# Kernel optimization log

Hardware: AMD Instinct MI355X
Metric: run time of the kernel (lower is better)

Reference implementation:

```python
import jax, jax.numpy as jnp
import numpy as np

# config (mirrors the original `config` module)
V = 50257   # vocab_size
E = 512     # embedding dim
H = 1024    # hidden size
S = 128     # encoder length
B = 8       # config.beam_size
T = 64      # config.MAX_LENGTH
SOS = 1
EOS = 2
NEG = -1e9


def setup_inputs() -> dict:
    key = jax.random.key(0)
    ks = jax.random.split(key, 7)
    s = jnp.float32(0.05)
    return {
        "emb": jax.random.normal(ks[0], (V, E), jnp.float32) * s,
        "Wx": jax.random.normal(ks[1], (E, 3 * H), jnp.float32) * s,
        "Wh": jax.random.normal(ks[2], (H, 3 * H), jnp.float32) * s,
        "W_out": jax.random.normal(ks[3], (2 * H, V), jnp.float32) * s,
        "b_out": jax.random.normal(ks[4], (V,), jnp.float32) * s,
        "enc": jax.random.normal(ks[5], (S, H), jnp.float32) * s,
        "h0": jax.random.normal(ks[6], (H,), jnp.float32) * s,
    }


def _gru(x, h, Wx, Wh):
    gx = x @ Wx
    gh = h @ Wh
    xz, xr, xn = jnp.split(gx, 3, axis=-1)
    hz, hr, hn = jnp.split(gh, 3, axis=-1)
    z = jax.nn.sigmoid(xz + hz)
    r = jax.nn.sigmoid(xr + hr)
    n = jnp.tanh(xn + r * hn)
    return (1.0 - z) * n + z * h


def _beam_search(emb, Wx, Wh, W_out, b_out, enc, h0):
    def step(carry, step_idx):
        tokens, cum, length, finished, latest, h = carry
        # decoder step for all live beams at once (batch = B)
        x = emb[latest]                               # [B, E]
        h_new = _gru(x, h, Wx, Wh)                    # [B, H]
        att = jax.nn.softmax(h_new @ enc.T, axis=-1)  # [B, S]
        ctx = att @ enc                               # [B, H]
        logits = jnp.concatenate([h_new, ctx], axis=-1) @ W_out + b_out
        logp = jax.nn.log_softmax(logits, axis=-1)    # [B, V] == log(probs)
        tk_lp, tk_id = jax.lax.top_k(logp, B)         # per-beam topk(beam_size)

        alive = ~finished
        # candidate cumulative log-probs and lengths (length counts SOS, as in avg_log_prob)
        cand_cum = cum[:, None] + jnp.where(alive[:, None], tk_lp, 0.0)   # [B, B]
        cand_len = length[:, None] + alive[:, None].astype(jnp.int32)    # [B, B]
        cand_score = cand_cum / cand_len.astype(cand_cum.dtype)          # avg_log_prob
        # finished beams contribute a single frozen candidate (their result slot)
        valid = alive[:, None] | (jnp.arange(B)[None, :] == 0)
        # steps == 0: num_old_beams = 1 (only beam 0 expands)
        valid = valid & ((step_idx > 0) | (jnp.arange(B)[:, None] == 0))
        flat = jnp.where(valid, cand_score, NEG).reshape(-1)             # [B*B]
        _, top_idx = jax.lax.top_k(flat, B)           # sort_beams + keep beam_size
        parent = top_idx // B
        child = top_idx % B

        p_fin = finished[parent]
        p_len = length[parent]
        new_tok = tk_id[parent, child]                # [B]
        # append new token at position (len - 1) unless parent already finished
        pos = (jnp.arange(T)[None, :] == (p_len - 1)[:, None]) & (~p_fin)[:, None]
        tokens_n = jnp.where(pos, new_tok[:, None], tokens[parent])
        fin_n = p_fin | (new_tok == EOS)
        cum_n = cand_cum.reshape(-1)[top_idx]
        len_n = cand_len.reshape(-1)[top_idx]
        latest_n = jnp.where(p_fin, latest[parent], new_tok)
        return (tokens_n, cum_n, len_n, fin_n, latest_n, h_new[parent]), None

    tokens0 = jnp.zeros((B, T), jnp.int32)
    cum0 = jnp.zeros((B,), jnp.float32)       # log_probs = [0.0] for SOS
    len0 = jnp.ones((B,), jnp.int32)          # tokens = [SOS]
    fin0 = jnp.zeros((B,), bool)
    latest0 = jnp.full((B,), SOS, jnp.int32)
    h_init = jnp.tile(h0[None, :], (B, 1))
    carry = (tokens0, cum0, len0, fin0, latest0, h_init)
    (tokens, cum, length, finished, _, _), _ = jax.lax.scan(step, carry, jnp.arange(T))

    score = cum / length.astype(cum.dtype)
    # prefer finished (EOS) beams, else fall back to live beams, best avg_log_prob
    adj = jnp.where(jnp.any(finished), jnp.where(finished, score, NEG), score)
    best = jnp.argmax(adj)
    return tokens[best], score[best]


def reference(emb, Wx, Wh, W_out, b_out, enc, h0):
    return _beam_search(emb, Wx, Wh, W_out, b_out, enc, h0)
```

## Files before the change

### kernel.cpp

```cpp
#include <hip/hip_runtime.h>
#include <math.h>

#define V    50257
#define E    512
#define H    1024
#define S    128
#define BS   8
#define T    64
#define SOS  1
#define EOS  2
#define NEGV (-1e9f)
#define H3   (3*H)
#define KS   16
#define RPK  ((E+H)/KS)
#define TKCH 6283
#define CB   197

__global__ void k_init(const float* __restrict__ h0, float* h, float* cum,
                       int* len, int* fin, int* lat, int* tok) {
    int t = threadIdx.x;
    for (int i = t; i < BS*H; i += 256) h[i] = h0[i % H];
    for (int i = t; i < BS*T; i += 256) tok[i] = 0;
    if (t < BS) { cum[t] = 0.f; len[t] = 1; fin[t] = 0; lat[t] = SOS; }
}

__global__ __launch_bounds__(256) void k_gru_part(
    const float* __restrict__ emb, const float* __restrict__ Wx,
    const float* __restrict__ Wh, const float* __restrict__ h,
    const int* __restrict__ lat, float* __restrict__ part)
{
    int jb = blockIdx.x;
    int k  = blockIdx.y;
    int t  = threadIdx.x;
    int j  = jb*256 + t;
    int c0 = k * RPK;
    __shared__ float vals[RPK*BS];
    for (int m = t; m < RPK*8; m += 256) {
        int c = c0 + (m >> 3);
        int b = m & 7;
        float v;
        if (c < E) v = emb[(size_t)lat[b]*E + c];
        else       v = h[b*H + (c - E)];
        vals[m] = v;
    }
    __syncthreads();
    float pz[BS] = {0}, pr[BS] = {0}, pnx[BS] = {0}, pnh[BS] = {0};
    for (int cc = 0; cc < RPK; ++cc) {
        int c = c0 + cc;
        bool isx = (c < E);
        const float* Wrow = isx ? (Wx + (size_t)c*H3) : (Wh + (size_t)(c-E)*H3);
        float wz = Wrow[j];
        float wr = Wrow[j + H];
        float wn = Wrow[j + 2*H];
        #pragma unroll
        for (int b = 0; b < BS; ++b) {
            float v = vals[cc*8 + b];
            pz[b] += v * wz;
            pr[b] += v * wr;
            if (isx) pnx[b] += v * wn; else pnh[b] += v * wn;
        }
    }
    #pragma unroll
    for (int b = 0; b < BS; ++b) {
        part[(((size_t)k*4 + 0)*8 + b)*H + j] = pz[b];
        part[(((size_t)k*4 + 1)*8 + b)*H + j] = pr[b];
        part[(((size_t)k*4 + 2)*8 + b)*H + j] = pnx[b];
        part[(((size_t)k*4 + 3)*8 + b)*H + j] = pnh[b];
    }
}

__global__ __launch_bounds__(256) void k_gate_attn(
    const float* __restrict__ part, const float* __restrict__ h,
    const float* __restrict__ enc, float* __restrict__ hcT)
{
    int b = blockIdx.x;
    int t = threadIdx.x;
    __shared__ float hn[H];
    __shared__ float att[S];
    __shared__ float smax, ssum;
    for (int j = t; j < H; j += 256) {
        float pz = 0.f, pr = 0.f, pnx = 0.f, pnh = 0.f;
        #pragma unroll
        for (int k = 0; k < KS; ++k) {
            pz  += part[(((size_t)k*4 + 0)*8 + b)*H + j];
            pr  += part[(((size_t)k*4 + 1)*8 + b)*H + j];
            pnx += part[(((size_t)k*4 + 2)*8 + b)*H + j];
            pnh += part[(((size_t)k*4 + 3)*8 + b)*H + j];
        }
        float z = 1.f / (1.f + expf(-pz));
        float r = 1.f / (1.f + expf(-pr));
        float n = tanhf(pnx + r * pnh);
        float v = (1.f - z) * n + z * h[b*H + j];
        hn[j] = v;
        hcT[(size_t)j*8 + b] = v;
    }
    __syncthreads();
    int wave = t >> 6, lane = t & 63;
    for (int s = wave; s < S; s += 4) {
        float acc = 0.f;
        #pragma unroll 4
        for (int hh = lane; hh < H; hh += 64)
            acc += hn[hh] * enc[(size_t)s*H + hh];
        #pragma unroll
        for (int off = 32; off; off >>= 1) acc += __shfl_down(acc, off, 64);
        if (lane == 0) att[s] = acc;
    }
    __syncthreads();
    if (t == 0) {
        float m = -3.0e38f;
        for (int s = 0; s < S; ++s) m = fmaxf(m, att[s]);
        smax = m;
    }
    __syncthreads();
    if (t < S) att[t] = expf(att[t] - smax);
    __syncthreads();
    if (t == 0) {
        float sum = 0.f;
        for (int s = 0; s < S; ++s) sum += att[s];
        ssum = sum;
    }
    __syncthreads();
    if (t < S) att[t] = att[t] / ssum;
    __syncthreads();
    for (int j = t; j < H; j += 256) {
        float acc = 0.f;
        for (int s = 0; s < S; ++s) acc += att[s] * enc[(size_t)s*H + j];
        hcT[(size_t)(H + j)*8 + b] = acc;
    }
}

__global__ __launch_bounds__(256) void k_gemv_part(
    const float* __restrict__ Wout, const float* __restrict__ hcT,
    float* __restrict__ lpart)
{
    int t  = threadIdx.x;
    int rs = blockIdx.y;
    int r0 = rs * 256;
    int c  = blockIdx.x * 256 + t;
    __shared__ float hc[256*8];
    for (int m = t; m < 256*8; m += 256) hc[m] = hcT[(size_t)r0*8 + m];
    __syncthreads();
    int cl = (c < V) ? c : (V - 1);
    const float* wp = Wout + (size_t)r0*V + cl;
    float a[8] = {0,0,0,0,0,0,0,0};
    #pragma unroll 8
    for (int rr = 0; rr < 256; ++rr) {
        float w = wp[(size_t)rr*V];
        const float* hr = hc + rr*8;
        #pragma unroll
        for (int b = 0; b < 8; ++b) a[b] += hr[b] * w;
    }
    if (c < V) {
        #pragma unroll
        for (int b = 0; b < 8; ++b)
            lpart[((size_t)rs*8 + b)*V + c] = a[b];
    }
}

__global__ __launch_bounds__(256) void k_topk_part(
    const float* __restrict__ lpart, const float* __restrict__ bout,
    float* __restrict__ cand_v, int* __restrict__ cand_i,
    float* __restrict__ cm, float* __restrict__ clp)
{
    int b = blockIdx.x, c = blockIdx.y, t = threadIdx.x;
    int vstart = c * TKCH;
    int vend = (vstart + TKCH < V) ? (vstart + TKCH) : V;
    float bv[8]; int bi[8];
    #pragma unroll
    for (int r = 0; r < 8; ++r) { bv[r] = -3.0e38f; bi[r] = 0x7fffffff; }
    float m = -3.0e38f, l = 0.f;
    for (int v = vstart + t; v < vend; v += 256) {
        float x = bout[v];
        #pragma unroll
        for (int r = 0; r < 8; ++r)
            x += lpart[((size_t)r*8 + b)*V + v];
        if (x > m) { l = l * expf(m - x) + 1.f; m = x; }
        else         l += expf(x - m);
        if (x > bv[7]) {
            bv[7] = x; bi[7] = v;
            #pragma unroll
            for (int q = 7; q > 0; --q) {
                if (bv[q] > bv[q-1]) {
                    float tv = bv[q]; bv[q] = bv[q-1]; bv[q-1] = tv;
                    int   ti = bi[q]; bi[q] = bi[q-1]; bi[q-1] = ti;
                }
            }
        }
    }
    __shared__ float pm[256], pl[256];
    pm[t] = m; pl[t] = l;
    __syncthreads();
    for (int off = 128; off; off >>= 1) {
        if (t < off) {
            float m2 = pm[t+off], l2 = pl[t+off];
            float M = fmaxf(pm[t], m2);
            pl[t] = pl[t]*expf(pm[t]-M) + l2*expf(m2-M);
            pm[t] = M;
        }
        __syncthreads();
    }
    if (t == 0) { cm[b*8 + c] = pm[0]; clp[b*8 + c] = pl[0]; }

    __shared__ float pv[2048];
    __shared__ int   pi[2048];
    __shared__ float rv[256];
    __shared__ int   ri[256], rp[256];
    #pragma unroll
    for (int r = 0; r < 8; ++r) { pv[t*8+r] = bv[r]; pi[t*8+r] = bi[r]; }
    __syncthreads();
    for (int round = 0; round < 8; ++round) {
        float lv = -3.0e38f; int li = 0x7fffffff, lp = -1;
        #pragma unroll
        for (int r = 0; r < 8; ++r) {
            float v2 = pv[t*8+r]; int i2 = pi[t*8+r];
            if (v2 > lv || (v2 == lv && i2 < li)) { lv = v2; li = i2; lp = t*8+r; }
        }
        rv[t] = lv; ri[t] = li; rp[t] = lp;
        __syncthreads();
        for (int off = 128; off; off >>= 1) {
            if (t < off) {
                if (rv[t+off] > rv[t] || (rv[t+off] == rv[t] && ri[t+off] < ri[t])) {
                    rv[t] = rv[t+off]; ri[t] = ri[t+off]; rp[t] = rp[t+off];
                }
            }
            __syncthreads();
        }
        if (t == 0) {
            cand_v[(b*8 + c)*8 + round] = rv[0];
            cand_i[(b*8 + c)*8 + round] = ri[0];
            pv[rp[0]] = -3.0e38f; pi[rp[0]] = 0x7fffffff;
        }
        __syncthreads();
    }
}

__global__ __launch_bounds__(256) void k_merge_update_fb(
    const float* __restrict__ cand_v, const int* __restrict__ cand_i,
    const float* __restrict__ cm, const float* __restrict__ clp,
    const float* cum_i, const int* len_i, const int* fin_i,
    const int* lat_i, const int* tok_i,
    float* cum_o, int* len_o, int* fin_o, int* lat_o, int* tok_o,
    const float* __restrict__ hcT, float* __restrict__ h, int step)
{
    int t = threadIdx.x;
    __shared__ float cv[512];
    __shared__ int   ci[512];
    __shared__ float t8v[64];
    __shared__ int   t8i[64];
    __shared__ float lse[8];
    for (int i = t; i < 512; i += 256) { cv[i] = cand_v[i]; ci[i] = cand_i[i]; }
    __syncthreads();
    if (t < 8) {
        int b = t;
        float m = -3.0e38f, l = 0.f;
        for (int c = 0; c < 8; ++c) {
            float m2 = cm[b*8 + c], l2 = clp[b*8 + c];
            float M = fmaxf(m, m2);
            l = l*expf(m - M) + l2*expf(m2 - M);
            m = M;
        }
        lse[b] = m + logf(l);
        unsigned long long tk = 0ull;
        for (int round = 0; round < 8; ++round) {
            float bvv = -3.4e38f; int bii = 0x7fffffff, bp = 0;
            for (int i = 0; i < 64; ++i) {
                if ((tk >> i) & 1ull) continue;
                float v2 = cv[b*64 + i]; int i2 = ci[b*64 + i];
                if (v2 > bvv || (v2 == bvv && i2 < bii)) { bvv = v2; bii = i2; bp = i; }
            }
            tk |= 1ull << bp;
            t8v[b*8 + round] = bvv;
            t8i[b*8 + round] = bii;
        }
    }
    __syncthreads();

    __shared__ float flat[64];
    __shared__ float ccum[64];
    __shared__ int   clen[64];
    __shared__ int   sel[8];
    if (t < 64) {
        int b = t >> 3, j = t & 7;
        int alive = fin_i[b] ? 0 : 1;
        float lp = t8v[b*8 + j] - lse[b];
        float cc = cum_i[b] + (alive ? lp : 0.f);
        int   cln = len_i[b] + alive;
        float score = cc / (float)cln;
        bool valid = (alive || j == 0) && ((step > 0) || (b == 0));
        flat[t] = valid ? score : NEGV;
        ccum[t] = cc; clen[t] = cln;
    }
    __syncthreads();
    if (t == 0) {
        unsigned long long tk = 0ull;
        for (int r = 0; r < 8; ++r) {
            float bestv = -3.4e38f; int bidx = 0;
            for (int i = 0; i < 64; ++i) {
                if (!((tk >> i) & 1ull) && flat[i] > bestv) { bestv = flat[i]; bidx = i; }
            }
            tk |= 1ull << bidx; sel[r] = bidx;
        }
    }
    __syncthreads();
    if (t < 8) {
        int idx = sel[t];
        int parent = idx >> 3, child = idx & 7;
        int p_fin = fin_i[parent];
        int new_tok = t8i[parent*8 + child];
        cum_o[t] = ccum[idx];
        len_o[t] = clen[idx];
        fin_o[t] = (p_fin || new_tok == EOS) ? 1 : 0;
        lat_o[t] = p_fin ? lat_i[parent] : new_tok;
    }
    __syncthreads();
    for (int m = t; m < BS*T; m += 256) {
        int nb = m / T, pos = m % T;
        int idx = sel[nb];
        int parent = idx >> 3, child = idx & 7;
        int p_fin = fin_i[parent];
        int p_len = len_i[parent];
        int new_tok = t8i[parent*8 + child];
        int val = tok_i[parent*T + pos];
        if (pos == p_len - 1 && !p_fin) val = new_tok;
        tok_o[m] = val;
    }
    for (int m = t; m < BS*H; m += 256) {
        int nb = m / H, j = m % H;
        int parent = sel[nb] >> 3;
        h[m] = hcT[(size_t)j*8 + parent];
    }
}

__global__ void k_final(const float* cum, const int* len, const int* fin,
                        const int* tok, float* out)
{
    int t = threadIdx.x;
    __shared__ int bestIdx;
    if (t == 0) {
        bool anyf = false;
        for (int b = 0; b < BS; ++b) anyf = anyf || (fin[b] != 0);
        float bestv = -3.4e38f; int bi_ = 0;
        for (int b = 0; b < BS; ++b) {
            float sc = cum[b] / (float)len[b];
            float adj = anyf ? (fin[b] ? sc : NEGV) : sc;
            if (adj > bestv) { bestv = adj; bi_ = b; }
        }
        bestIdx = bi_;
        out[T] = cum[bi_] / (float)len[bi_];
    }
    __syncthreads();
    if (t < T) out[t] = (float)tok[bestIdx*T + t];
}

extern "C" void kernel_launch(void* const* d_in, const int* in_sizes, int n_in,
                              void* d_out, int out_size, void* d_ws, size_t ws_size,
                              hipStream_t stream) {
    const float* emb  = (const float*)d_in[0];
    const float* Wx   = (const float*)d_in[1];
    const float* Wh   = (const float*)d_in[2];
    const float* Wout = (const float*)d_in[3];
    const float* bout = (const float*)d_in[4];
    const float* enc  = (const float*)d_in[5];
    const float* h0   = (const float*)d_in[6];
    float* out = (float*)d_out;

    char* w = (char*)d_ws;
    auto alloc = [&](size_t bytes) -> char* {
        char* p = w; w += (bytes + 255) & ~(size_t)255; return p;
    };

    float* h      = (float*)alloc((size_t)BS*H*4);
    float* hcT    = (float*)alloc((size_t)2*H*BS*4);
    float* part   = (float*)alloc((size_t)KS*4*BS*H*4);
    float* cumb0  = (float*)alloc(8*4);
    float* cumb1  = (float*)alloc(8*4);
    int* lenb0 = (int*)alloc(8*4);
    int* lenb1 = (int*)alloc(8*4);
    int* finb0 = (int*)alloc(8*4);
    int* finb1 = (int*)alloc(8*4);
    int* latb0 = (int*)alloc(8*4);
    int* latb1 = (int*)alloc(8*4);
    int* tokb0 = (int*)alloc((size_t)BS*T*4);
    int* tokb1 = (int*)alloc((size_t)BS*T*4);

    float* lpart  = (float*)alloc((size_t)8*BS*V*4);
    float* cand_v = (float*)alloc(8*8*8*4);
    int*   cand_i = (int*)  alloc(8*8*8*4);
    float* cm     = (float*)alloc(64*4);
    float* clp    = (float*)alloc(64*4);

    float* cumb[2] = {cumb0, cumb1};
    int*   lenb[2] = {lenb0, lenb1};
    int*   finb[2] = {finb0, finb1};
    int*   latb[2] = {latb0, latb1};
    int*   tokb[2] = {tokb0, tokb1};

    k_init<<<1, 256, 0, stream>>>(h0, h, cumb[0], lenb[0], finb[0], latb[0], tokb[0]);

    for (int s = 0; s < T; ++s) {
        int p = s & 1, q = 1 - p;
        k_gru_part<<<dim3(4, KS), 256, 0, stream>>>(emb, Wx, Wh, h, latb[p], part);
        k_gate_attn<<<BS, 256, 0, stream>>>(part, h, enc, hcT);
        k_gemv_part<<<dim3(CB, 8), 256, 0, stream>>>(Wout, hcT, lpart);
        k_gemv_part<<<dim3(CB, 8), 256, 0, stream>>>(Wout, hcT, lpart);
        k_topk_part<<<dim3(BS, 8), 256, 0, stream>>>(lpart, bout, cand_v, cand_i, cm, clp);
        k_merge_update_fb<<<1, 256, 0, stream>>>(cand_v, cand_i, cm, clp,
                                                 cumb[p], lenb[p], finb[p], latb[p], tokb[p],
                                                 cumb[q], lenb[q], finb[q], latb[q], tokb[q],
                                                 hcT, h, s);
    }
    k_final<<<1, 64, 0, stream>>>(cumb[0], lenb[0], finb[0], tokb[0], out);
}
```

Before: 26.80 ms.

## Fuse beam-search steps into one cooperative persistent kernel with grid syncs

Replaces the per-step chain of kernel launches with a single cooperative kernel that runs all 64 decode steps and separates stages with grid-wide syncs. It keeps a multi-kernel fallback if the cooperative launch fails. It also drops the duplicated output GEMV launch, splits the context computation out of the attention stage so it runs across 32 blocks instead of 8, and uses nontemporal loads for W_out. The aim is to remove launch overhead and redundant work, at the cost of many grid barriers per step. Stages with few blocks, such as merge, leave most of the grid idle.

New measurement: 61.89 ms. 2.31x slower.

```diff
diff --git a/kernel.cpp b/kernel.cpp
--- a/kernel.cpp
+++ b/kernel.cpp
@@ -1,5 +1,8 @@
 #include <hip/hip_runtime.h>
+#include <hip/hip_cooperative_groups.h>
 #include <math.h>
+
+namespace cg = cooperative_groups;
 
 #define V    50257
 #define E    512
@@ -15,32 +18,37 @@
 #define RPK  ((E+H)/KS)
 #define TKCH 6283
 #define CB   197
-
-__global__ void k_init(const float* __restrict__ h0, float* h, float* cum,
-                       int* len, int* fin, int* lat, int* tok) {
-    int t = threadIdx.x;
-    for (int i = t; i < BS*H; i += 256) h[i] = h0[i % H];
-    for (int i = t; i < BS*T; i += 256) tok[i] = 0;
-    if (t < BS) { cum[t] = 0.f; len[t] = 1; fin[t] = 0; lat[t] = SOS; }
-}
-
-__global__ __launch_bounds__(256) void k_gru_part(
-    const float* __restrict__ emb, const float* __restrict__ Wx,
-    const float* __restrict__ Wh, const float* __restrict__ h,
-    const int* __restrict__ lat, float* __restrict__ part)
-{
-    int jb = blockIdx.x;
-    int k  = blockIdx.y;
-    int t  = threadIdx.x;
-    int j  = jb*256 + t;
+#define SMB  21504
+
+struct Params {
+    const float *emb, *Wx, *Wh, *Wout, *bout, *enc, *h0;
+    float *out;
+    float *h, *hcT, *part, *lpart, *attg, *cand_v, *cm, *clp;
+    int   *cand_i;
+    float *cum0, *cum1;
+    int *len0, *len1, *fin0, *fin1, *lat0, *lat1, *tok0, *tok1;
+};
+
+
+__device__ __forceinline__ void init_body(const Params& p) {
+    int t = threadIdx.x;
+    for (int i = t; i < BS*H; i += 256) p.h[i] = p.h0[i % H];
+    for (int i = t; i < BS*T; i += 256) p.tok0[i] = 0;
+    if (t < BS) { p.cum0[t] = 0.f; p.len0[t] = 1; p.fin0[t] = 0; p.lat0[t] = SOS; }
+}
+
+__device__ __forceinline__ void gru_body(const Params& p, char* sm, int jb, int k,
+                                         const int* __restrict__ lat) {
+    int t = threadIdx.x;
+    int j = jb*256 + t;
     int c0 = k * RPK;
-    __shared__ float vals[RPK*BS];
+    float* vals = (float*)sm;
     for (int m = t; m < RPK*8; m += 256) {
         int c = c0 + (m >> 3);
         int b = m & 7;
         float v;
-        if (c < E) v = emb[(size_t)lat[b]*E + c];
-        else       v = h[b*H + (c - E)];
+        if (c < E) v = p.emb[(size_t)lat[b]*E + c];
+        else       v = p.h[b*H + (c - E)];
         vals[m] = v;
     }
     __syncthreads();
@@ -48,7 +56,7 @@
     for (int cc = 0; cc < RPK; ++cc) {
         int c = c0 + cc;
         bool isx = (c < E);
-        const float* Wrow = isx ? (Wx + (size_t)c*H3) : (Wh + (size_t)(c-E)*H3);
+        const float* Wrow = isx ? (p.Wx + (size_t)c*H3) : (p.Wh + (size_t)(c-E)*H3);
         float wz = Wrow[j];
         float wr = Wrow[j + H];
         float wn = Wrow[j + 2*H];
@@ -62,90 +70,92 @@
     }
     #pragma unroll
     for (int b = 0; b < BS; ++b) {
-        part[(((size_t)k*4 + 0)*8 + b)*H + j] = pz[b];
-        part[(((size_t)k*4 + 1)*8 + b)*H + j] = pr[b];
-        part[(((size_t)k*4 + 2)*8 + b)*H + j] = pnx[b];
-        part[(((size_t)k*4 + 3)*8 + b)*H + j] = pnh[b];
-    }
-}
-
-__global__ __launch_bounds__(256) void k_gate_attn(
-    const float* __restrict__ part, const float* __restrict__ h,
-    const float* __restrict__ enc, float* __restrict__ hcT)
-{
-    int b = blockIdx.x;
-    int t = threadIdx.x;
-    __shared__ float hn[H];
-    __shared__ float att[S];
-    __shared__ float smax, ssum;
+        p.part[(((size_t)k*4 + 0)*8 + b)*H + j] = pz[b];
+        p.part[(((size_t)k*4 + 1)*8 + b)*H + j] = pr[b];
+        p.part[(((size_t)k*4 + 2)*8 + b)*H + j] = pnx[b];
+        p.part[(((size_t)k*4 + 3)*8 + b)*H + j] = pnh[b];
+    }
+    __syncthreads();
+}
+
+__device__ __forceinline__ void gateA_body(const Params& p, char* sm, int b) {
+    int t = threadIdx.x;
+    float* hn   = (float*)sm;
+    float* att  = hn + H;
+    float* smax = att + S;
+    float* ssum = smax + 1;
     for (int j = t; j < H; j += 256) {
         float pz = 0.f, pr = 0.f, pnx = 0.f, pnh = 0.f;
         #pragma unroll
         for (int k = 0; k < KS; ++k) {
-            pz  += part[(((size_t)k*4 + 0)*8 + b)*H + j];
-            pr  += part[(((size_t)k*4 + 1)*8 + b)*H + j];
-            pnx += part[(((size_t)k*4 + 2)*8 + b)*H + j];
-            pnh += part[(((size_t)k*4 + 3)*8 + b)*H + j];
+            pz  += p.part[(((size_t)k*4 + 0)*8 + b)*H + j];
+            pr  += p.part[(((size_t)k*4 + 1)*8 + b)*H + j];
+            pnx += p.part[(((size_t)k*4 + 2)*8 + b)*H + j];
+            pnh += p.part[(((size_t)k*4 + 3)*8 + b)*H + j];
         }
         float z = 1.f / (1.f + expf(-pz));
         float r = 1.f / (1.f + expf(-pr));
         float n = tanhf(pnx + r * pnh);
-        float v = (1.f - z) * n + z * h[b*H + j];
+        float v = (1.f - z) * n + z * p.h[b*H + j];
         hn[j] = v;
-        hcT[(size_t)j*8 + b] = v;
+        p.hcT[(size_t)j*8 + b] = v;
     }
     __syncthreads();
     int wave = t >> 6, lane = t & 63;
-    for (int s = wave; s < S; s += 4) {
+    for (int s2 = wave; s2 < S; s2 += 4) {
         float acc = 0.f;
         #pragma unroll 4
         for (int hh = lane; hh < H; hh += 64)
-            acc += hn[hh] * enc[(size_t)s*H + hh];
+            acc += hn[hh] * p.enc[(size_t)s2*H + hh];
         #pragma unroll
         for (int off = 32; off; off >>= 1) acc += __shfl_down(acc, off, 64);
-        if (lane == 0) att[s] = acc;
+        if (lane == 0) att[s2] = acc;
     }
     __syncthreads();
     if (t == 0) {
         float m = -3.0e38f;
-        for (int s = 0; s < S; ++s) m = fmaxf(m, att[s]);
-        smax = m;
-    }
-    __syncthreads();
-    if (t < S) att[t] = expf(att[t] - smax);
+        for (int s2 = 0; s2 < S; ++s2) m = fmaxf(m, att[s2]);
+        *smax = m;
+    }
+    __syncthreads();
+    if (t < S) att[t] = expf(att[t] - *smax);
     __syncthreads();
     if (t == 0) {
         float sum = 0.f;
-        for (int s = 0; s < S; ++s) sum += att[s];
-        ssum = sum;
-    }
-    __syncthreads();
-    if (t < S) att[t] = att[t] / ssum;
-    __syncthreads();
-    for (int j = t; j < H; j += 256) {
-        float acc = 0.f;
-        for (int s = 0; s < S; ++s) acc += att[s] * enc[(size_t)s*H + j];
-        hcT[(size_t)(H + j)*8 + b] = acc;
-    }
-}
-
-__global__ __launch_bounds__(256) void k_gemv_part(
-    const float* __restrict__ Wout, const float* __restrict__ hcT,
-    float* __restrict__ lpart)
-{
-    int t  = threadIdx.x;
-    int rs = blockIdx.y;
+        for (int s2 = 0; s2 < S; ++s2) sum += att[s2];
+        *ssum = sum;
+    }
+    __syncthreads();
+    if (t < S) { att[t] = att[t] / *ssum; p.attg[b*S + t] = att[t]; }
+    __syncthreads();
+}
+
+__device__ __forceinline__ void ctx_body(const Params& p, char* sm, int vb) {
+    int t = threadIdx.x;
+    int b = vb & 7, jc = vb >> 3;
+    float* att = (float*)sm;
+    if (t < S) att[t] = p.attg[b*S + t];
+    __syncthreads();
+    int j = jc*256 + t;
+    float acc = 0.f;
+    for (int s2 = 0; s2 < S; ++s2) acc += att[s2] * p.enc[(size_t)s2*H + j];
+    p.hcT[(size_t)(H + j)*8 + b] = acc;
+    __syncthreads();
+}
+
+__device__ __forceinline__ void gemv_body(const Params& p, char* sm, int cb, int rs) {
+    int t = threadIdx.x;
     int r0 = rs * 256;
-    int c  = blockIdx.x * 256 + t;
-    __shared__ float hc[256*8];
-    for (int m = t; m < 256*8; m += 256) hc[m] = hcT[(size_t)r0*8 + m];
+    int c  = cb*256 + t;
+    float* hc = (float*)sm;
+    for (int m = t; m < 256*8; m += 256) hc[m] = p.hcT[(size_t)r0*8 + m];
     __syncthreads();
     int cl = (c < V) ? c : (V - 1);
-    const float* wp = Wout + (size_t)r0*V + cl;
+    const float* wp = p.Wout + (size_t)r0*V + cl;
     float a[8] = {0,0,0,0,0,0,0,0};
     #pragma unroll 8
     for (int rr = 0; rr < 256; ++rr) {
-        float w = wp[(size_t)rr*V];
+        float w = __builtin_nontemporal_load(wp + (size_t)rr*V);
         const float* hr = hc + rr*8;
         #pragma unroll
         for (int b = 0; b < 8; ++b) a[b] += hr[b] * w;
@@ -153,16 +163,21 @@
     if (c < V) {
         #pragma unroll
         for (int b = 0; b < 8; ++b)
-            lpart[((size_t)rs*8 + b)*V + c] = a[b];
-    }
-}
-
-__global__ __launch_bounds__(256) void k_topk_part(
-    const float* __restrict__ lpart, const float* __restrict__ bout,
-    float* __restrict__ cand_v, int* __restrict__ cand_i,
-    float* __restrict__ cm, float* __restrict__ clp)
-{
-    int b = blockIdx.x, c = blockIdx.y, t = threadIdx.x;
+            p.lpart[((size_t)rs*8 + b)*V + c] = a[b];
+    }
+    __syncthreads();
+}
+
+__device__ __forceinline__ void topk_body(const Params& p, char* sm, int b, int c) {
+    int t = threadIdx.x;
+    float* pm = (float*)(sm);
+    float* pl = (float*)(sm + 1024);
+    float* pv = (float*)(sm + 2048);
+    int*   pi = (int*)  (sm + 10240);
+    float* rv = (float*)(sm + 18432);
+    int*   ri = (int*)  (sm + 19456);
+    int*   rp = (int*)  (sm + 20480);
+
     int vstart = c * TKCH;
     int vend = (vstart + TKCH < V) ? (vstart + TKCH) : V;
     float bv[8]; int bi[8];
@@ -170,10 +185,10 @@
     for (int r = 0; r < 8; ++r) { bv[r] = -3.0e38f; bi[r] = 0x7fffffff; }
     float m = -3.0e38f, l = 0.f;
     for (int v = vstart + t; v < vend; v += 256) {
-        float x = bout[v];
+        float x = p.bout[v];
         #pragma unroll
         for (int r = 0; r < 8; ++r)
-            x += lpart[((size_t)r*8 + b)*V + v];
+            x += p.lpart[((size_t)r*8 + b)*V + v];
         if (x > m) { l = l * expf(m - x) + 1.f; m = x; }
         else         l += expf(x - m);
         if (x > bv[7]) {
@@ -187,7 +202,6 @@
             }
         }
     }
-    __shared__ float pm[256], pl[256];
     pm[t] = m; pl[t] = l;
     __syncthreads();
     for (int off = 128; off; off >>= 1) {
@@ -199,12 +213,8 @@
         }
         __syncthreads();
     }
-    if (t == 0) { cm[b*8 + c] = pm[0]; clp[b*8 + c] = pl[0]; }
-
-    __shared__ float pv[2048];
-    __shared__ int   pi[2048];
-    __shared__ float rv[256];
-    __shared__ int   ri[256], rp[256];
+    if (t == 0) { p.cm[b*8 + c] = pm[0]; p.clp[b*8 + c] = pl[0]; }
+
     #pragma unroll
     for (int r = 0; r < 8; ++r) { pv[t*8+r] = bv[r]; pi[t*8+r] = bi[r]; }
     __syncthreads();
@@ -226,35 +236,38 @@
             __syncthreads();
         }
         if (t == 0) {
-            cand_v[(b*8 + c)*8 + round] = rv[0];
-            cand_i[(b*8 + c)*8 + round] = ri[0];
+            p.cand_v[(b*8 + c)*8 + round] = rv[0];
+            p.cand_i[(b*8 + c)*8 + round] = ri[0];
             pv[rp[0]] = -3.0e38f; pi[rp[0]] = 0x7fffffff;
         }
         __syncthreads();
     }
-}
-
-__global__ __launch_bounds__(256) void k_merge_update_fb(
-    const float* __restrict__ cand_v, const int* __restrict__ cand_i,
-    const float* __restrict__ cm, const float* __restrict__ clp,
+    __syncthreads();
+}
+
+__device__ __forceinline__ void merge_body(const Params& p, char* sm,
     const float* cum_i, const int* len_i, const int* fin_i,
     const int* lat_i, const int* tok_i,
-    float* cum_o, int* len_o, int* fin_o, int* lat_o, int* tok_o,
-    const float* __restrict__ hcT, float* __restrict__ h, int step)
+    float* cum_o, int* len_o, int* fin_o, int* lat_o, int* tok_o, int step)
 {
     int t = threadIdx.x;
-    __shared__ float cv[512];
-    __shared__ int   ci[512];
-    __shared__ float t8v[64];
-    __shared__ int   t8i[64];
-    __shared__ float lse[8];
-    for (int i = t; i < 512; i += 256) { cv[i] = cand_v[i]; ci[i] = cand_i[i]; }
+    float* cv   = (float*)(sm);
+    int*   ci   = (int*)  (sm + 2048);
+    float* t8v  = (float*)(sm + 4096);
+    int*   t8i  = (int*)  (sm + 4352);
+    float* lse  = (float*)(sm + 4608);
+    float* flat = (float*)(sm + 4640);
+    float* ccum = (float*)(sm + 4896);
+    int*   clen = (int*)  (sm + 5152);
+    int*   sel  = (int*)  (sm + 5408);
+
+    for (int i = t; i < 512; i += 256) { cv[i] = p.cand_v[i]; ci[i] = p.cand_i[i]; }
     __syncthreads();
     if (t < 8) {
         int b = t;
         float m = -3.0e38f, l = 0.f;
         for (int c = 0; c < 8; ++c) {
-            float m2 = cm[b*8 + c], l2 = clp[b*8 + c];
+            float m2 = p.cm[b*8 + c], l2 = p.clp[b*8 + c];
             float M = fmaxf(m, m2);
             l = l*expf(m - M) + l2*expf(m2 - M);
             m = M;
@@ -274,11 +287,6 @@
         }
     }
     __syncthreads();
-
-    __shared__ float flat[64];
-    __shared__ float ccum[64];
-    __shared__ int   clen[64];
-    __shared__ int   sel[8];
     if (t < 64) {
         int b = t >> 3, j = t & 7;
         int alive = fin_i[b] ? 0 : 1;
@@ -314,8 +322,8 @@
     }
     __syncthreads();
     for (int m = t; m < BS*T; m += 256) {
-        int nb = m / T, pos = m % T;
-        int idx = sel[nb];
+        int nb2 = m / T, pos = m % T;
+        int idx = sel[nb2];
         int parent = idx >> 3, child = idx & 7;
         int p_fin = fin_i[parent];
         int p_len = len_i[parent];
@@ -325,89 +333,161 @@
         tok_o[m] = val;
     }
     for (int m = t; m < BS*H; m += 256) {
-        int nb = m / H, j = m % H;
-        int parent = sel[nb] >> 3;
-        h[m] = hcT[(size_t)j*8 + parent];
-    }
-}
-
-__global__ void k_final(const float* cum, const int* len, const int* fin,
-                        const int* tok, float* out)
-{
-    int t = threadIdx.x;
-    __shared__ int bestIdx;
+        int nb2 = m / H, j = m % H;
+        int parent = sel[nb2] >> 3;
+        p.h[m] = p.hcT[(size_t)j*8 + parent];
+    }
+    __syncthreads();
+}
+
+__device__ __forceinline__ void final_body(const Params& p, char* sm) {
+    int t = threadIdx.x;
+    int* bestIdx = (int*)sm;
     if (t == 0) {
         bool anyf = false;
-        for (int b = 0; b < BS; ++b) anyf = anyf || (fin[b] != 0);
+        for (int b = 0; b < BS; ++b) anyf = anyf || (p.fin0[b] != 0);
         float bestv = -3.4e38f; int bi_ = 0;
         for (int b = 0; b < BS; ++b) {
-            float sc = cum[b] / (float)len[b];
-            float adj = anyf ? (fin[b] ? sc : NEGV) : sc;
+            float sc = p.cum0[b] / (float)p.len0[b];
+            float adj = anyf ? (p.fin0[b] ? sc : NEGV) : sc;
             if (adj > bestv) { bestv = adj; bi_ = b; }
         }
-        bestIdx = bi_;
-        out[T] = cum[bi_] / (float)len[bi_];
-    }
-    __syncthreads();
-    if (t < T) out[t] = (float)tok[bestIdx*T + t];
+        *bestIdx = bi_;
+        p.out[T] = p.cum0[bi_] / (float)p.len0[bi_];
+    }
+    __syncthreads();
+    if (t < T) p.out[t] = (float)p.tok0[*bestIdx*T + t];
+}
+
+__global__ __launch_bounds__(256, 2) void k_all(Params p) {
+    cg::grid_group grid = cg::this_grid();
+    __shared__ __align__(16) char sm[SMB];
+    int bid = blockIdx.x, nb = gridDim.x;
+
+    if (bid == 0) init_body(p);
+    grid.sync();
+
+    for (int s = 0; s < T; ++s) {
+        int pp = s & 1;
+        const float* cum_i = pp ? p.cum1 : p.cum0;
+        float*       cum_o = pp ? p.cum0 : p.cum1;
+        const int* len_i = pp ? p.len1 : p.len0;  int* len_o = pp ? p.len0 : p.len1;
+        const int* fin_i = pp ? p.fin1 : p.fin0;  int* fin_o = pp ? p.fin0 : p.fin1;
+        const int* lat_i = pp ? p.lat1 : p.lat0;  int* lat_o = pp ? p.lat0 : p.lat1;
+        const int* tok_i = pp ? p.tok1 : p.tok0;  int* tok_o = pp ? p.tok0 : p.tok1;
+
+        for (int vb = bid; vb < 64; vb += nb)      gru_body(p, sm, vb & 3, vb >> 2, lat_i);
+        grid.sync();
+        for (int vb = bid; vb < 8; vb += nb)       gateA_body(p, sm, vb);
+        grid.sync();
+        for (int vb = bid; vb < 32; vb += nb)      ctx_body(p, sm, vb);
+        grid.sync();
+        for (int vb = bid; vb < CB*8; vb += nb)    gemv_body(p, sm, vb % CB, vb / CB);
+        grid.sync();
+        for (int vb = bid; vb < 64; vb += nb)      topk_body(p, sm, vb & 7, vb >> 3);
+        grid.sync();
+        if (bid == 0) merge_body(p, sm, cum_i, len_i, fin_i, lat_i, tok_i,
+                                 cum_o, len_o, fin_o, lat_o, tok_o, s);
+        grid.sync();
+    }
+    if (bid == 0) final_body(p, sm);
+}
+
+__global__ void k_init_s(Params p) { init_body(p); }
+__global__ __launch_bounds__(256) void k_gru_s(Params p, int s) {
+    __shared__ __align__(16) char sm[3072];
+    const int* lat = (s & 1) ? p.lat1 : p.lat0;
+    gru_body(p, sm, blockIdx.x, blockIdx.y, lat);
+}
+__global__ __launch_bounds__(256) void k_gate_s(Params p) {
+    __shared__ __align__(16) char sm[4624];
+    gateA_body(p, sm, blockIdx.x);
+}
+__global__ __launch_bounds__(256) void k_ctx_s(Params p) {
+    __shared__ __align__(16) char sm[512];
+    ctx_body(p, sm, blockIdx.x);
+}
+__global__ __launch_bounds__(256) void k_gemv_s(Params p) {
+    __shared__ __align__(16) char sm[8192];
+    gemv_body(p, sm, blockIdx.x, blockIdx.y);
+}
+__global__ __launch_bounds__(256) void k_topk_s(Params p) {
+    __shared__ __align__(16) char sm[SMB];
+    topk_body(p, sm, blockIdx.x, blockIdx.y);
+}
+__global__ __launch_bounds__(256) void k_merge_s(Params p, int s) {
+    __shared__ __align__(16) char sm[5440];
+    int pp = s & 1;
+    merge_body(p, sm,
+               pp ? p.cum1 : p.cum0, pp ? p.len1 : p.len0, pp ? p.fin1 : p.fin0,
+               pp ? p.lat1 : p.lat0, pp ? p.tok1 : p.tok0,
+               pp ? p.cum0 : p.cum1, pp ? p.len0 : p.len1, pp ? p.fin0 : p.fin1,
+               pp ? p.lat0 : p.lat1, pp ? p.tok0 : p.tok1, s);
+}
+__global__ void k_final_s(Params p) {
+    __shared__ __align__(16) char sm[16];
+    final_body(p, sm);
 }
 
 extern "C" void kernel_launch(void* const* d_in, const int* in_sizes, int n_in,
                               void* d_out, int out_size, void* d_ws, size_t ws_size,
                               hipStream_t stream) {
-    const float* emb  = (const float*)d_in[0];
-    const float* Wx   = (const float*)d_in[1];
-    const float* Wh   = (const float*)d_in[2];
-    const float* Wout = (const float*)d_in[3];
-    const float* bout = (const float*)d_in[4];
-    const float* enc  = (const float*)d_in[5];
-    const float* h0   = (const float*)d_in[6];
-    float* out = (float*)d_out;
+    Params p;
+    p.emb  = (const float*)d_in[0];
+    p.Wx   = (const float*)d_in[1];
+    p.Wh   = (const float*)d_in[2];
+    p.Wout = (const float*)d_in[3];
+    p.bout = (const float*)d_in[4];
+    p.enc  = (const float*)d_in[5];
+    p.h0   = (const float*)d_in[6];
+    p.out  = (float*)d_out;
 
     char* w = (char*)d_ws;
     auto alloc = [&](size_t bytes) -> char* {
-        char* p = w; w += (bytes + 255) & ~(size_t)255; return p;
+        char* q = w; w += (bytes + 255) & ~(size_t)255; return q;
     };
 
-    float* h      = (float*)alloc((size_t)BS*H*4);
-    float* hcT    = (float*)alloc((size_t)2*H*BS*4);
-    float* part   = (float*)alloc((size_t)KS*4*BS*H*4);
-    float* cumb0  = (float*)alloc(8*4);
-    float* cumb1  = (float*)alloc(8*4);
-    int* lenb0 = (int*)alloc(8*4);
-    int* lenb1 = (int*)alloc(8*4);
-    int* finb0 = (int*)alloc(8*4);
-    int* finb1 = (int*)alloc(8*4);
-    int* latb0 = (int*)alloc(8*4);
-    int* latb1 = (int*)alloc(8*4);
-    int* tokb0 = (int*)alloc((size_t)BS*T*4);
-    int* tokb1 = (int*)alloc((size_t)BS*T*4);
-
-    float* lpart  = (float*)alloc((size_t)8*BS*V*4);
-    float* cand_v = (float*)alloc(8*8*8*4);
-    int*   cand_i = (int*)  alloc(8*8*8*4);
-    float* cm     = (float*)alloc(64*4);
-    float* clp    = (float*)alloc(64*4);
-
-    float* cumb[2] = {cumb0, cumb1};
-    int*   lenb[2] = {lenb0, lenb1};
-    int*   finb[2] = {finb0, finb1};
-    int*   latb[2] = {latb0, latb1};
-    int*   tokb[2] = {tokb0, tokb1};
-
-    k_init<<<1, 256, 0, stream>>>(h0, h, cumb[0], lenb[0], finb[0], latb[0], tokb[0]);
-
-    for (int s = 0; s < T; ++s) {
-        int p = s & 1, q = 1 - p;
-        k_gru_part<<<dim3(4, KS), 256, 0, stream>>>(emb, Wx, Wh, h, latb[p], part);
-        k_gate_attn<<<BS, 256, 0, stream>>>(part, h, enc, hcT);
-        k_gemv_part<<<dim3(CB, 8), 256, 0, stream>>>(Wout, hcT, lpart);
-        k_gemv_part<<<dim3(CB, 8), 256, 0, stream>>>(Wout, hcT, lpart);
-        k_topk_part<<<dim3(BS, 8), 256, 0, stream>>>(lpart, bout, cand_v, cand_i, cm, clp);
-        k_merge_update_fb<<<1, 256, 0, stream>>>(cand_v, cand_i, cm, clp,
-                                                 cumb[p], lenb[p], finb[p], latb[p], tokb[p],
-                                                 cumb[q], lenb[q], finb[q], latb[q], tokb[q],
-                                                 hcT, h, s);
-    }
-    k_final<<<1, 64, 0, stream>>>(cumb[0], lenb[0], finb[0], tokb[0], out);
-}
+    p.h    = (float*)alloc((size_t)BS*H*4);
+    p.hcT  = (float*)alloc((size_t)2*H*BS*4);
+    p.part = (float*)alloc((size_t)KS*4*BS*H*4);
+    p.attg = (float*)alloc((size_t)BS*S*4);
+    p.cum0 = (float*)alloc(8*4);
+    p.cum1 = (float*)alloc(8*4);
+    p.len0 = (int*)alloc(8*4);  p.len1 = (int*)alloc(8*4);
+    p.fin0 = (int*)alloc(8*4);  p.fin1 = (int*)alloc(8*4);
+    p.lat0 = (int*)alloc(8*4);  p.lat1 = (int*)alloc(8*4);
+    p.tok0 = (int*)alloc((size_t)BS*T*4);
+    p.tok1 = (int*)alloc((size_t)BS*T*4);
+    p.lpart  = (float*)alloc((size_t)8*BS*V*4);
+    p.cand_v = (float*)alloc(8*8*8*4);
+    p.cand_i = (int*)  alloc(8*8*8*4);
+    p.cm     = (float*)alloc(64*4);
+    p.clp    = (float*)alloc(64*4);
+
+    bool coop = false;
+    int maxb = 0;
+    hipError_t oe = hipOccupancyMaxActiveBlocksPerMultiprocessor(&maxb, k_all, 256, 0);
+    if (oe == hipSuccess && maxb >= 1) {
+        int grid = maxb * 256;
+        if (grid > 1024) grid = 1024;
+        if (grid < 256)  grid = 256;
+        void* args[] = { (void*)&p };
+        hipError_t le = hipLaunchCooperativeKernel((const void*)k_all,
+                                                   dim3(grid), dim3(256),
+                                                   args, 0, stream);
+        if (le == hipSuccess) coop = true;
+    }
+
+    if (!coop) {
+        k_init_s<<<1, 256, 0, stream>>>(p);
+        for (int s = 0; s < T; ++s) {
+            k_gru_s <<<dim3(4, KS), 256, 0, stream>>>(p, s);
+            k_gate_s<<<BS,          256, 0, stream>>>(p);
+            k_ctx_s <<<32,          256, 0, stream>>>(p);
+            k_gemv_s<<<dim3(CB, 8), 256, 0, stream>>>(p);
+            k_topk_s<<<dim3(BS, 8), 256, 0, stream>>>(p);
+            k_merge_s<<<1,          256, 0, stream>>>(p, s);
+        }
+        k_final_s<<<1, 64, 0, stream>>>(p);
+    }
+}
```
